# Kernel tuning notes

Measured on AMD Instinct MI355X. Metric: run time of the kernel, lower is better.

Reference implementation:

```python
import jax, jax.numpy as jnp
import numpy as np

FP4_VALUES = jnp.array([0.0, 0.5, 1.0, 1.5, 2.0, 3.0, 4.0, 6.0,
                        -0.0, -0.5, -1.0, -1.5, -2.0, -3.0, -4.0, -6.0], dtype=jnp.float32)
ALPHA = 1.702
LIMIT = 7.0


def convert_moe_packed_tensors(blocks, scales):
    """Dequantize MXFP4: blocks [E, R, G, 16] packed nibbles, scales [E, R, G] biased exponents.
    Returns [E, G*32, R] fp32 (transposed like the torch reference)."""
    lo = FP4_VALUES[blocks & 0x0F]          # even output positions
    hi = FP4_VALUES[(blocks >> 4) & 0x0F]   # odd output positions
    vals = jnp.stack([lo, hi], axis=-1).reshape(*blocks.shape[:-1], 32)  # [E,R,G,32] interleaved
    scale = jnp.exp2((scales - 127).astype(jnp.float32))                 # 2**(s-127)
    w = vals * scale[..., None]
    E, R = blocks.shape[0], blocks.shape[1]
    return w.reshape(E, R, -1).transpose(0, 2, 1)  # [E, G*32, R]


def setup_inputs() -> dict:
    key = jax.random.key(0)
    ks = jax.random.split(key, 8)
    E, H, I = 8, 2880, 2880
    B, S = 1, 1024
    hidden_states = jax.random.normal(ks[0], (B, S, H), dtype=jnp.float32)
    routing_weights = jax.random.uniform(ks[1], (B * S, E), dtype=jnp.float32)
    gate_up_proj_blocks = jax.random.randint(ks[2], (E, 2 * I, H // 32, 16), 0, 256, dtype=jnp.int32)
    gate_up_proj_scales = jax.random.randint(ks[3], (E, 2 * I, H // 32), 118, 130, dtype=jnp.int32)
    gate_up_proj_bias = jax.random.normal(ks[4], (E, 2 * I), dtype=jnp.float32)
    down_proj_blocks = jax.random.randint(ks[5], (E, H, I // 32, 16), 0, 256, dtype=jnp.int32)
    down_proj_scales = jax.random.randint(ks[6], (E, H, I // 32), 118, 130, dtype=jnp.int32)
    down_proj_bias = jax.random.normal(ks[7], (E, H), dtype=jnp.float32)
    return {
        "hidden_states": hidden_states,
        "routing_weights": routing_weights,
        "gate_up_proj_blocks": gate_up_proj_blocks,
        "gate_up_proj_scales": gate_up_proj_scales,
        "gate_up_proj_bias": gate_up_proj_bias,
        "down_proj_blocks": down_proj_blocks,
        "down_proj_scales": down_proj_scales,
        "down_proj_bias": down_proj_bias,
    }


def reference(hidden_states, routing_weights, gate_up_proj_blocks, gate_up_proj_scales,
              gate_up_proj_bias, down_proj_blocks, down_proj_scales, down_proj_bias):
    B, S, H = hidden_states.shape
    gate_up_proj = convert_moe_packed_tensors(gate_up_proj_blocks, gate_up_proj_scales)  # [E, H, 2I]
    down_proj = convert_moe_packed_tensors(down_proj_blocks, down_proj_scales)           # [E, I, H]
    x = hidden_states.reshape(-1, H)                                                     # [T, H]
    # dense all-expert GLU MLP
    gate_up = jnp.einsum('th,ehf->etf', x, gate_up_proj) + gate_up_proj_bias[:, None, :]  # [E, T, 2I]
    gate = jnp.minimum(gate_up[..., ::2], LIMIT)
    up = jnp.clip(gate_up[..., 1::2], -LIMIT, LIMIT)
    glu = gate * jax.nn.sigmoid(gate * ALPHA)
    nxt = jnp.einsum('eti,eih->eth', (up + 1.0) * glu, down_proj) + down_proj_bias[:, None, :]  # [E, T, H]
    nxt = nxt * routing_weights.T[:, :, None]   # weight each expert's output per token
    out = nxt.sum(axis=0).reshape(B, S, H)
    return out
```

## Files before the change

### kernel.cpp

```cpp
#include <hip/hip_runtime.h>
#include <cstdint>


typedef float  floatx4 __attribute__((ext_vector_type(4)));
typedef __bf16 bf16x8  __attribute__((ext_vector_type(8)));

#define E8   8
#define Hdim 2880
#define Idim 2880
#define Ttok 1024
#define R1   5760
#define Gg   90
#define K2   (E8 * Idim)

__device__ __forceinline__ void load_lds16(const void* gptr, void* lptr) {
  __builtin_amdgcn_global_load_lds(
      (const __attribute__((address_space(1))) uint32_t*)gptr,
      (__attribute__((address_space(3))) uint32_t*)lptr, 16, 0, 0);
}

__device__ __forceinline__ uint32_t f2bf(float f) {
  uint32_t u = __float_as_uint(f);
  return (u + 0x7FFFu + ((u >> 16) & 1u)) >> 16;
}

__device__ __forceinline__ uint32_t perm(uint32_t hi, uint32_t lo, uint32_t sel) {
  return __builtin_amdgcn_perm(hi, lo, sel);
}

struct DqLut { uint32_t Ll, Lh, Hl, Hh; };

__device__ __forceinline__ DqLut make_lut(int s) {
  uint32_t A  = ((uint32_t)(s - 127) << 7) & 0xFFFFu;
  uint32_t e1 = (0x3F00u + A) & 0xFFFFu, e2 = (0x3F80u + A) & 0xFFFFu;
  uint32_t e3 = (0x3FC0u + A) & 0xFFFFu, e4 = (0x4000u + A) & 0xFFFFu;
  uint32_t e5 = (0x4040u + A) & 0xFFFFu, e6 = (0x4080u + A) & 0xFFFFu;
  uint32_t e7 = (0x40C0u + A) & 0xFFFFu;
  uint32_t B01 = e1 << 16, B23 = e2 | (e3 << 16);
  uint32_t B45 = e4 | (e5 << 16), B67 = e6 | (e7 << 16);
  DqLut L;
  L.Ll = perm(B23, B01, 0x06040200u);
  L.Hl = perm(B23, B01, 0x07050301u);
  L.Lh = perm(B67, B45, 0x06040200u);
  L.Hh = perm(B67, B45, 0x07050301u);
  return L;
}

__device__ __forceinline__ uint4 dq8(const DqLut& L, int4 wr) {
  uint32_t p = perm((uint32_t)wr.y, (uint32_t)wr.x, 0x04000400u);
  uint32_t q = perm((uint32_t)wr.w, (uint32_t)wr.z, 0x04000400u);
  uint32_t w = perm(q, p, 0x05040100u);
  uint32_t ilo = w & 0x07070707u;
  uint32_t ihi = (w >> 4) & 0x07070707u;
  uint32_t Llo = perm(L.Lh, L.Ll, ilo);
  uint32_t Hlo = perm(L.Hh, L.Hl, ilo) | ((w << 4) & 0x80808080u);
  uint32_t Lhi = perm(L.Lh, L.Ll, ihi);
  uint32_t Hhi = perm(L.Hh, L.Hl, ihi) | (w & 0x80808080u);
  uint32_t t0 = perm(Hlo, Llo, 0x05010400u);
  uint32_t t1 = perm(Hlo, Llo, 0x07030602u);
  uint32_t t2 = perm(Hhi, Lhi, 0x05010400u);
  uint32_t t3 = perm(Hhi, Lhi, 0x07030602u);
  uint4 o;
  o.x = perm(t2, t0, 0x05040100u);
  o.y = perm(t2, t0, 0x07060302u);
  o.z = perm(t3, t1, 0x05040100u);
  o.w = perm(t3, t1, 0x07060302u);
  return o;
}

__global__ void cvt_x_kernel(const float* __restrict__ x, uint16_t* __restrict__ xb, int n) {
  int i = (blockIdx.x * 256 + threadIdx.x) * 4;
  if (i >= n) return;
  float4 v = *(const float4*)(x + i);
  ushort4 o = make_ushort4((uint16_t)f2bf(v.x), (uint16_t)f2bf(v.y),
                           (uint16_t)f2bf(v.z), (uint16_t)f2bf(v.w));
  *(ushort4*)(xb + i) = o;
}

__global__ void dq_w_kernel(const int* __restrict__ blocks, const int* __restrict__ scales,
                            uint16_t* __restrict__ wd) {
  size_t q = (size_t)blockIdx.x * 256 + threadIdx.x;
  size_t g = q >> 2;
  int part = (int)(q & 3);
  int4 w = ((const int4*)(blocks + g * 16))[part];
  DqLut L = make_lut(scales[g]);
  *(uint4*)(wd + g * 32 + part * 8) = dq8(L, w);
}

__global__ void dq_w2t_kernel(const int* __restrict__ blocks, const int* __restrict__ scales,
                              uint16_t* __restrict__ wt) {
  size_t q = (size_t)blockIdx.x * 256 + threadIdx.x;
  size_t g = q >> 2;
  int part = (int)(q & 3);
  int e  = (int)(g / ((size_t)Hdim * Gg));
  int rm = (int)(g % ((size_t)Hdim * Gg));
  int h  = rm / Gg;
  int ig = rm % Gg;
  int4 w = ((const int4*)(blocks + g * 16))[part];
  DqLut L = make_lut(scales[g]);
  *(uint4*)(wt + ((size_t)h * E8 + e) * Idim + (size_t)ig * 32 + part * 8) = dq8(L, w);
}

__global__ void bias_init_kernel(const float* __restrict__ rw, const float* __restrict__ bias,
                                 float* __restrict__ out) {
  int t  = blockIdx.y;
  int h4 = (blockIdx.x * 256 + threadIdx.x) * 4;
  if (h4 >= Hdim) return;
  float4 s = make_float4(0.f, 0.f, 0.f, 0.f);
  #pragma unroll
  for (int e = 0; e < E8; ++e) {
    float w = rw[t * E8 + e];
    float4 b = *(const float4*)(bias + (size_t)e * Hdim + h4);
    s.x += w * b.x; s.y += w * b.y; s.z += w * b.z; s.w += w * b.w;
  }
  *(float4*)(out + (size_t)t * Hdim + h4) = s;
}

__global__ __launch_bounds__(512) void gemm1_dp_kernel(
    const uint16_t* __restrict__ xb, const uint16_t* __restrict__ w1d,
    const float* __restrict__ bias, const float* __restrict__ rw,
    uint16_t* __restrict__ act) {
  extern __shared__ uint16_t smem[];
  uint16_t* sAr = smem;
  uint16_t* sBr = smem + 3 * 8192;
  const int tid  = threadIdx.x;
  const int lane = tid & 63, wv = tid >> 6;
  const int wm = wv >> 1, wn = wv & 1;
  const int col = lane & 15, quad = lane >> 4;
  const int e  = blockIdx.z;
  const int t0 = blockIdx.x * 256;
  const int i0 = blockIdx.y * 64;

  floatx4 acc[4][4] = {};

  const uint16_t* aSrc0;
  const uint16_t* aSrc1;
  const uint16_t* bSrc;
  {
    int L0 = tid;
    int r0 = L0 >> 2;
    int g0 = (L0 & 3) ^ ((r0 >> 1) & 3);
    aSrc0 = xb + (size_t)(t0 + r0) * Hdim + g0 * 8;
    int L1 = 512 + tid;
    int r1 = L1 >> 2;
    int g1 = (L1 & 3) ^ ((r1 >> 1) & 3);
    aSrc1 = xb + (size_t)(t0 + r1) * Hdim + g1 * 8;
    int rb = tid >> 2;
    int gb = (tid & 3) ^ ((rb >> 1) & 3);
    int orig = 2 * (((rb >> 6) << 5) + (rb & 31)) + ((rb >> 5) & 1);
    bSrc = w1d + ((size_t)e * R1 + 2 * i0 + orig) * Hdim + gb * 8;
  }
  const int aOff0 = (wv * 64) * 8;
  const int aOff1 = (512 + wv * 64) * 8;
  const int bOff  = (wv * 64) * 8;

  auto STAGE = [&](int kt, int slot) {
    const int k0 = kt * 32;
    uint16_t* A = sAr + slot * 8192;
    uint16_t* B = sBr + slot * 4096;
    load_lds16(aSrc0 + k0, A + aOff0);
    load_lds16(aSrc1 + k0, A + aOff1);
    load_lds16(bSrc + k0, B + bOff);
  };

  STAGE(0, 0);
  STAGE(1, 1);

  int sr = 0;
  for (int j = 0; j < 90; ++j) {
    asm volatile("s_waitcnt vmcnt(3)" ::: "memory");
    __builtin_amdgcn_s_barrier();
    asm volatile("" ::: "memory");
    int js = j + 2; if (js > 89) js = 89;
    int sw = sr + 2; if (sw >= 3) sw -= 3;
    STAGE(js, sw);

    const uint16_t* A = sAr + sr * 8192;
    const uint16_t* B = sBr + sr * 4096;
    bf16x8 af[4], bfr[4];
    #pragma unroll
    for (int fm = 0; fm < 4; ++fm) {
      int row = wm * 64 + fm * 16 + col;
      int g = quad ^ ((row >> 1) & 3);
      af[fm] = *(const bf16x8*)&A[row * 32 + g * 8];
    }
    #pragma unroll
    for (int fn = 0; fn < 4; ++fn) {
      int row = wn * 64 + fn * 16 + col;
      int g = quad ^ ((row >> 1) & 3);
      bfr[fn] = *(const bf16x8*)&B[row * 32 + g * 8];
    }
    __builtin_amdgcn_s_setprio(1);
    #pragma unroll
    for (int fm = 0; fm < 4; ++fm)
      #pragma unroll
      for (int fn = 0; fn < 4; ++fn)
        acc[fm][fn] = __builtin_amdgcn_mfma_f32_16x16x32_bf16(
            af[fm], bfr[fn], acc[fm][fn], 0, 0, 0);
    __builtin_amdgcn_s_setprio(0);
    sr = (sr + 1 == 3) ? 0 : sr + 1;
  }

  #pragma unroll
  for (int fm = 0; fm < 4; ++fm) {
    #pragma unroll
    for (int p = 0; p < 2; ++p) {
      floatx4 ga = acc[fm][p], ua = acc[fm][p + 2];
      int ig = i0 + wn * 32 + p * 16 + col;
      float bg = bias[(size_t)e * R1 + 2 * ig];
      float bu = bias[(size_t)e * R1 + 2 * ig + 1];
      #pragma unroll
      for (int r = 0; r < 4; ++r) {
        int t = t0 + wm * 64 + fm * 16 + quad * 4 + r;
        float gate = fminf(ga[r] + bg, 7.0f);
        float up   = fminf(fmaxf(ua[r] + bu, -7.0f), 7.0f);
        float glu  = gate / (1.0f + __expf(-1.702f * gate));
        float a    = rw[t * E8 + e] * (up + 1.0f) * glu;
        act[((size_t)t * E8 + e) * Idim + ig] = (uint16_t)f2bf(a);
      }
    }
  }
}

__global__ __launch_bounds__(512) void gemm2_dp_kernel(
    const uint16_t* __restrict__ actT, const uint16_t* __restrict__ w2t,
    float* __restrict__ out) {
  extern __shared__ uint16_t smem[];
  uint16_t* sAr = smem;
  uint16_t* sBr = smem + 3 * 8192;
  const int tid  = threadIdx.x;
  const int lane = tid & 63, wv = tid >> 6;
  const int wm = wv >> 1, wn = wv & 1;
  const int col = lane & 15, quad = lane >> 4;
  const int t0 = blockIdx.x * 256;
  const int h0 = blockIdx.y * 128;
  const int kbase = blockIdx.z * (K2 / 8);

  floatx4 acc[4][4] = {};

  const uint16_t* aSrc0;
  const uint16_t* aSrc1;
  const uint16_t* bSrc;
  {
    int L0 = tid;
    int r0 = L0 >> 2;
    int g0 = (L0 & 3) ^ ((r0 >> 1) & 3);
    aSrc0 = actT + (size_t)(t0 + r0) * K2 + kbase + g0 * 8;
    int L1 = 512 + tid;
    int r1 = L1 >> 2;
    int g1 = (L1 & 3) ^ ((r1 >> 1) & 3);
    aSrc1 = actT + (size_t)(t0 + r1) * K2 + kbase + g1 * 8;
    int rb = tid >> 2;
    int gb = (tid & 3) ^ ((rb >> 1) & 3);
    int hb = h0 + rb; if (hb > Hdim - 1) hb = Hdim - 1;
    bSrc = w2t + (size_t)hb * K2 + kbase + gb * 8;
  }
  const int aOff0 = (wv * 64) * 8;
  const int aOff1 = (512 + wv * 64) * 8;
  const int bOff  = (wv * 64) * 8;

  auto STAGE = [&](int kt, int slot) {
    const int k0 = kt * 32;
    uint16_t* A = sAr + slot * 8192;
    uint16_t* B = sBr + slot * 4096;
    load_lds16(aSrc0 + k0, A + aOff0);
    load_lds16(aSrc1 + k0, A + aOff1);
    load_lds16(bSrc + k0, B + bOff);
  };

  STAGE(0, 0);
  STAGE(1, 1);

  int sr = 0;
  for (int j = 0; j < 90; ++j) {
    asm volatile("s_waitcnt vmcnt(3)" ::: "memory");
    __builtin_amdgcn_s_barrier();
    asm volatile("" ::: "memory");
    int js = j + 2; if (js > 89) js = 89;
    int sw = sr + 2; if (sw >= 3) sw -= 3;
    STAGE(js, sw);

    const uint16_t* A = sAr + sr * 8192;
    const uint16_t* B = sBr + sr * 4096;
    bf16x8 af[4], bfr[4];
    #pragma unroll
    for (int fm = 0; fm < 4; ++fm) {
      int row = wm * 64 + fm * 16 + col;
      int g = quad ^ ((row >> 1) & 3);
      af[fm] = *(const bf16x8*)&A[row * 32 + g * 8];
    }
    #pragma unroll
    for (int fn = 0; fn < 4; ++fn) {
      int row = wn * 64 + fn * 16 + col;
      int g = quad ^ ((row >> 1) & 3);
      bfr[fn] = *(const bf16x8*)&B[row * 32 + g * 8];
    }
    __builtin_amdgcn_s_setprio(1);
    #pragma unroll
    for (int fm = 0; fm < 4; ++fm)
      #pragma unroll
      for (int fn = 0; fn < 4; ++fn)
        acc[fm][fn] = __builtin_amdgcn_mfma_f32_16x16x32_bf16(
            af[fm], bfr[fn], acc[fm][fn], 0, 0, 0);
    __builtin_amdgcn_s_setprio(0);
    sr = (sr + 1 == 3) ? 0 : sr + 1;
  }

  #pragma unroll
  for (int fm = 0; fm < 4; ++fm)
    #pragma unroll
    for (int fn = 0; fn < 4; ++fn) {
      int h = h0 + wn * 64 + fn * 16 + col;
      if (h < Hdim) {
        #pragma unroll
        for (int r = 0; r < 4; ++r) {
          int t = t0 + wm * 64 + fm * 16 + quad * 4 + r;
          atomicAdd(out + (size_t)t * Hdim + h, acc[fm][fn][r]);
        }
      }
    }
}

extern "C" void kernel_launch(void* const* d_in, const int* in_sizes, int n_in,
                              void* d_out, int out_size, void* d_ws, size_t ws_size,
                              hipStream_t stream) {
  (void)in_sizes; (void)n_in; (void)out_size; (void)ws_size;
  const float* x        = (const float*)d_in[0];
  const float* rw       = (const float*)d_in[1];
  const int*   gub_b    = (const int*)d_in[2];
  const int*   gub_s    = (const int*)d_in[3];
  const float* gub_bias = (const float*)d_in[4];
  const int*   dwn_b    = (const int*)d_in[5];
  const int*   dwn_s    = (const int*)d_in[6];
  const float* dwn_bias = (const float*)d_in[7];
  float* out = (float*)d_out;

  const size_t nXb  = (size_t)Ttok * Hdim;
  const size_t nAct = (size_t)Ttok * K2;
  const size_t nW1  = (size_t)E8 * R1 * Hdim;

  uint16_t* xb  = (uint16_t*)d_ws;
  uint16_t* act = xb + nXb;
  uint16_t* w1d = act + nAct;
  uint16_t* w2t = w1d + nW1;

  static int attr_set = 0;
  if (!attr_set) {
    (void)hipFuncSetAttribute((const void*)gemm1_dp_kernel,
                              hipFuncAttributeMaxDynamicSharedMemorySize, 73728);
    (void)hipFuncSetAttribute((const void*)gemm2_dp_kernel,
                              hipFuncAttributeMaxDynamicSharedMemorySize, 73728);
    attr_set = 1;
  }

  cvt_x_kernel<<<dim3((Ttok * Hdim / 4 + 255) / 256), 256, 0, stream>>>(x, xb, Ttok * Hdim);
  dq_w_kernel<<<dim3((int)((size_t)E8 * R1 * Gg * 4 / 256)), 256, 0, stream>>>(gub_b, gub_s, w1d);
  dq_w2t_kernel<<<dim3((int)((size_t)E8 * Hdim * Gg * 4 / 256)), 256, 0, stream>>>(dwn_b, dwn_s, w2t);
  bias_init_kernel<<<dim3(3, Ttok), 256, 0, stream>>>(rw, dwn_bias, out);
  gemm1_dp_kernel<<<dim3(4, 45, 8), 512, 73728, stream>>>(xb, w1d, gub_bias, rw, act);
  gemm2_dp_kernel<<<dim3(4, 23, 8), 512, 73728, stream>>>(act, w2t, out);
}
```

Baseline: 982.1 us.

## Halve GEMM block threads to 256 with 2-per-CU bounds and larger per-wave tiles

Both GEMM kernels now run 256 threads (4 waves) per block instead of 512. Each wave computes a 128x64 tile (8x4 MFMA fragments), so the block tile stays 256x128, and each thread issues 6 LDS-direct loads per stage instead of 3, with the vmcnt wait adjusted to match. Launch bounds request 2 blocks per CU. GEMM2's split-K grows from 8 to 12 slices, giving more blocks but more atomic adds to the output. Doubling accumulators per wave raises register pressure, and two 72 KB LDS blocks per CU may not fit, which would cap residency at one block.

Result: slower. 1.022 ms (+4.0%).

```diff
diff --git a/kernel.cpp b/kernel.cpp
--- a/kernel.cpp
+++ b/kernel.cpp
@@ -116,7 +116,7 @@
   *(float4*)(out + (size_t)t * Hdim + h4) = s;
 }
 
-__global__ __launch_bounds__(512) void gemm1_dp_kernel(
+__global__ __launch_bounds__(256, 2) void gemm1_dp_kernel(
     const uint16_t* __restrict__ xb, const uint16_t* __restrict__ w1d,
     const float* __restrict__ bias, const float* __restrict__ rw,
     uint16_t* __restrict__ act) {
@@ -131,36 +131,37 @@
   const int t0 = blockIdx.x * 256;
   const int i0 = blockIdx.y * 64;
 
-  floatx4 acc[4][4] = {};
-
-  const uint16_t* aSrc0;
-  const uint16_t* aSrc1;
-  const uint16_t* bSrc;
-  {
-    int L0 = tid;
-    int r0 = L0 >> 2;
-    int g0 = (L0 & 3) ^ ((r0 >> 1) & 3);
-    aSrc0 = xb + (size_t)(t0 + r0) * Hdim + g0 * 8;
-    int L1 = 512 + tid;
-    int r1 = L1 >> 2;
-    int g1 = (L1 & 3) ^ ((r1 >> 1) & 3);
-    aSrc1 = xb + (size_t)(t0 + r1) * Hdim + g1 * 8;
-    int rb = tid >> 2;
-    int gb = (tid & 3) ^ ((rb >> 1) & 3);
+  floatx4 acc[8][4] = {};
+
+  const uint16_t* aSrc[4];
+  const uint16_t* bSrc[2];
+  int aOff[4], bOff[2];
+  #pragma unroll
+  for (int q = 0; q < 4; ++q) {
+    int L = q * 256 + tid;
+    int r = L >> 2;
+    int g = (L & 3) ^ ((r >> 1) & 3);
+    aSrc[q] = xb + (size_t)(t0 + r) * Hdim + g * 8;
+    aOff[q] = (q * 256 + wv * 64) * 8;
+  }
+  #pragma unroll
+  for (int q = 0; q < 2; ++q) {
+    int L = q * 256 + tid;
+    int rb = L >> 2;
+    int gb = (L & 3) ^ ((rb >> 1) & 3);
     int orig = 2 * (((rb >> 6) << 5) + (rb & 31)) + ((rb >> 5) & 1);
-    bSrc = w1d + ((size_t)e * R1 + 2 * i0 + orig) * Hdim + gb * 8;
-  }
-  const int aOff0 = (wv * 64) * 8;
-  const int aOff1 = (512 + wv * 64) * 8;
-  const int bOff  = (wv * 64) * 8;
+    bSrc[q] = w1d + ((size_t)e * R1 + 2 * i0 + orig) * Hdim + gb * 8;
+    bOff[q] = (q * 256 + wv * 64) * 8;
+  }
 
   auto STAGE = [&](int kt, int slot) {
     const int k0 = kt * 32;
     uint16_t* A = sAr + slot * 8192;
     uint16_t* B = sBr + slot * 4096;
-    load_lds16(aSrc0 + k0, A + aOff0);
-    load_lds16(aSrc1 + k0, A + aOff1);
-    load_lds16(bSrc + k0, B + bOff);
+    #pragma unroll
+    for (int q = 0; q < 4; ++q) load_lds16(aSrc[q] + k0, A + aOff[q]);
+    #pragma unroll
+    for (int q = 0; q < 2; ++q) load_lds16(bSrc[q] + k0, B + bOff[q]);
   };
 
   STAGE(0, 0);
@@ -168,7 +169,7 @@
 
   int sr = 0;
   for (int j = 0; j < 90; ++j) {
-    asm volatile("s_waitcnt vmcnt(3)" ::: "memory");
+    asm volatile("s_waitcnt vmcnt(6)" ::: "memory");
     __builtin_amdgcn_s_barrier();
     asm volatile("" ::: "memory");
     int js = j + 2; if (js > 89) js = 89;
@@ -177,10 +178,10 @@
 
     const uint16_t* A = sAr + sr * 8192;
     const uint16_t* B = sBr + sr * 4096;
-    bf16x8 af[4], bfr[4];
-    #pragma unroll
-    for (int fm = 0; fm < 4; ++fm) {
-      int row = wm * 64 + fm * 16 + col;
+    bf16x8 af[8], bfr[4];
+    #pragma unroll
+    for (int fm = 0; fm < 8; ++fm) {
+      int row = wm * 128 + fm * 16 + col;
       int g = quad ^ ((row >> 1) & 3);
       af[fm] = *(const bf16x8*)&A[row * 32 + g * 8];
     }
@@ -192,7 +193,7 @@
     }
     __builtin_amdgcn_s_setprio(1);
     #pragma unroll
-    for (int fm = 0; fm < 4; ++fm)
+    for (int fm = 0; fm < 8; ++fm)
       #pragma unroll
       for (int fn = 0; fn < 4; ++fn)
         acc[fm][fn] = __builtin_amdgcn_mfma_f32_16x16x32_bf16(
@@ -202,7 +203,7 @@
   }
 
   #pragma unroll
-  for (int fm = 0; fm < 4; ++fm) {
+  for (int fm = 0; fm < 8; ++fm) {
     #pragma unroll
     for (int p = 0; p < 2; ++p) {
       floatx4 ga = acc[fm][p], ua = acc[fm][p + 2];
@@ -211,7 +212,7 @@
       float bu = bias[(size_t)e * R1 + 2 * ig + 1];
       #pragma unroll
       for (int r = 0; r < 4; ++r) {
-        int t = t0 + wm * 64 + fm * 16 + quad * 4 + r;
+        int t = t0 + wm * 128 + fm * 16 + quad * 4 + r;
         float gate = fminf(ga[r] + bg, 7.0f);
         float up   = fminf(fmaxf(ua[r] + bu, -7.0f), 7.0f);
         float glu  = gate / (1.0f + __expf(-1.702f * gate));
@@ -222,7 +223,7 @@
   }
 }
 
-__global__ __launch_bounds__(512) void gemm2_dp_kernel(
+__global__ __launch_bounds__(256, 2) void gemm2_dp_kernel(
     const uint16_t* __restrict__ actT, const uint16_t* __restrict__ w2t,
     float* __restrict__ out) {
   extern __shared__ uint16_t smem[];
@@ -234,58 +235,59 @@
   const int col = lane & 15, quad = lane >> 4;
   const int t0 = blockIdx.x * 256;
   const int h0 = blockIdx.y * 128;
-  const int kbase = blockIdx.z * (K2 / 8);
-
-  floatx4 acc[4][4] = {};
-
-  const uint16_t* aSrc0;
-  const uint16_t* aSrc1;
-  const uint16_t* bSrc;
-  {
-    int L0 = tid;
-    int r0 = L0 >> 2;
-    int g0 = (L0 & 3) ^ ((r0 >> 1) & 3);
-    aSrc0 = actT + (size_t)(t0 + r0) * K2 + kbase + g0 * 8;
-    int L1 = 512 + tid;
-    int r1 = L1 >> 2;
-    int g1 = (L1 & 3) ^ ((r1 >> 1) & 3);
-    aSrc1 = actT + (size_t)(t0 + r1) * K2 + kbase + g1 * 8;
-    int rb = tid >> 2;
-    int gb = (tid & 3) ^ ((rb >> 1) & 3);
+  const int kbase = blockIdx.z * (K2 / 12);
+
+  floatx4 acc[8][4] = {};
+
+  const uint16_t* aSrc[4];
+  const uint16_t* bSrc[2];
+  int aOff[4], bOff[2];
+  #pragma unroll
+  for (int q = 0; q < 4; ++q) {
+    int L = q * 256 + tid;
+    int r = L >> 2;
+    int g = (L & 3) ^ ((r >> 1) & 3);
+    aSrc[q] = actT + (size_t)(t0 + r) * K2 + kbase + g * 8;
+    aOff[q] = (q * 256 + wv * 64) * 8;
+  }
+  #pragma unroll
+  for (int q = 0; q < 2; ++q) {
+    int L = q * 256 + tid;
+    int rb = L >> 2;
+    int gb = (L & 3) ^ ((rb >> 1) & 3);
     int hb = h0 + rb; if (hb > Hdim - 1) hb = Hdim - 1;
-    bSrc = w2t + (size_t)hb * K2 + kbase + gb * 8;
-  }
-  const int aOff0 = (wv * 64) * 8;
-  const int aOff1 = (512 + wv * 64) * 8;
-  const int bOff  = (wv * 64) * 8;
+    bSrc[q] = w2t + (size_t)hb * K2 + kbase + gb * 8;
+    bOff[q] = (q * 256 + wv * 64) * 8;
+  }
 
   auto STAGE = [&](int kt, int slot) {
     const int k0 = kt * 32;
     uint16_t* A = sAr + slot * 8192;
     uint16_t* B = sBr + slot * 4096;
-    load_lds16(aSrc0 + k0, A + aOff0);
-    load_lds16(aSrc1 + k0, A + aOff1);
-    load_lds16(bSrc + k0, B + bOff);
+    #pragma unroll
+    for (int q = 0; q < 4; ++q) load_lds16(aSrc[q] + k0, A + aOff[q]);
+    #pragma unroll
+    for (int q = 0; q < 2; ++q) load_lds16(bSrc[q] + k0, B + bOff[q]);
   };
 
   STAGE(0, 0);
   STAGE(1, 1);
 
   int sr = 0;
-  for (int j = 0; j < 90; ++j) {
-    asm volatile("s_waitcnt vmcnt(3)" ::: "memory");
+  for (int j = 0; j < 60; ++j) {
+    asm volatile("s_waitcnt vmcnt(6)" ::: "memory");
     __builtin_amdgcn_s_barrier();
     asm volatile("" ::: "memory");
-    int js = j + 2; if (js > 89) js = 89;
+    int js = j + 2; if (js > 59) js = 59;
     int sw = sr + 2; if (sw >= 3) sw -= 3;
     STAGE(js, sw);
 
     const uint16_t* A = sAr + sr * 8192;
     const uint16_t* B = sBr + sr * 4096;
-    bf16x8 af[4], bfr[4];
-    #pragma unroll
-    for (int fm = 0; fm < 4; ++fm) {
-      int row = wm * 64 + fm * 16 + col;
+    bf16x8 af[8], bfr[4];
+    #pragma unroll
+    for (int fm = 0; fm < 8; ++fm) {
+      int row = wm * 128 + fm * 16 + col;
       int g = quad ^ ((row >> 1) & 3);
       af[fm] = *(const bf16x8*)&A[row * 32 + g * 8];
     }
@@ -297,7 +299,7 @@
     }
     __builtin_amdgcn_s_setprio(1);
     #pragma unroll
-    for (int fm = 0; fm < 4; ++fm)
+    for (int fm = 0; fm < 8; ++fm)
       #pragma unroll
       for (int fn = 0; fn < 4; ++fn)
         acc[fm][fn] = __builtin_amdgcn_mfma_f32_16x16x32_bf16(
@@ -307,14 +309,14 @@
   }
 
   #pragma unroll
-  for (int fm = 0; fm < 4; ++fm)
+  for (int fm = 0; fm < 8; ++fm)
     #pragma unroll
     for (int fn = 0; fn < 4; ++fn) {
       int h = h0 + wn * 64 + fn * 16 + col;
       if (h < Hdim) {
         #pragma unroll
         for (int r = 0; r < 4; ++r) {
-          int t = t0 + wm * 64 + fm * 16 + quad * 4 + r;
+          int t = t0 + wm * 128 + fm * 16 + quad * 4 + r;
           atomicAdd(out + (size_t)t * Hdim + h, acc[fm][fn][r]);
         }
       }
@@ -357,6 +359,6 @@
   dq_w_kernel<<<dim3((int)((size_t)E8 * R1 * Gg * 4 / 256)), 256, 0, stream>>>(gub_b, gub_s, w1d);
   dq_w2t_kernel<<<dim3((int)((size_t)E8 * Hdim * Gg * 4 / 256)), 256, 0, stream>>>(dwn_b, dwn_s, w2t);
   bias_init_kernel<<<dim3(3, Ttok), 256, 0, stream>>>(rw, dwn_bias, out);
-  gemm1_dp_kernel<<<dim3(4, 45, 8), 512, 73728, stream>>>(xb, w1d, gub_bias, rw, act);
-  gemm2_dp_kernel<<<dim3(4, 23, 8), 512, 73728, stream>>>(act, w2t, out);
-}
+  gemm1_dp_kernel<<<dim3(4, 45, 8), 256, 73728, stream>>>(xb, w1d, gub_bias, rw, act);
+  gemm2_dp_kernel<<<dim3(4, 23, 12), 256, 73728, stream>>>(act, w2t, out);
+}
```
